# Performance work log

Hardware: AMD Instinct MI355X
Metric: run time of the kernel (lower is better)

## Reference

```python
import jax, jax.numpy as jnp
import numpy as np

B, S, D, H, DFF = 2, 2048, 1024, 16, 4096
DK = D // H
EPS = 1e-6


def setup_inputs() -> dict:
    key = jax.random.key(0)
    ks = jax.random.split(key, 12)
    p = lambda k, shp: (jax.random.normal(k, shp, dtype=jnp.float32) * 0.02)
    return {
        "x": jax.random.normal(ks[0], (B, S, D), dtype=jnp.float32),
        "src_mask": jax.random.randint(ks[1], (B, 1, 1, S), 0, 2, dtype=jnp.int32),
        "wq": p(ks[2], (D, D)), "bq": jnp.zeros((D,), jnp.float32),
        "wk": p(ks[3], (D, D)), "bk": jnp.zeros((D,), jnp.float32),
        "wv": p(ks[4], (D, D)), "bv": jnp.zeros((D,), jnp.float32),
        "wo": p(ks[5], (D, D)), "bo": jnp.zeros((D,), jnp.float32),
        "w1": p(ks[6], (D, DFF)), "b1": jnp.zeros((DFF,), jnp.float32),
        "w2": p(ks[7], (DFF, D)), "b2": jnp.zeros((D,), jnp.float32),
        "a1": jnp.ones((1,), jnp.float32), "g1": jnp.zeros((1,), jnp.float32),
        "a2": jnp.ones((1,), jnp.float32), "g2": jnp.zeros((1,), jnp.float32),
    }


def _layernorm(x, alpha, bias):
    # Faithful to source: scalar alpha/bias, std with Bessel correction, eps on std
    mean = jnp.mean(x, axis=-1, keepdims=True)
    std = jnp.std(x, axis=-1, keepdims=True, ddof=1)
    return alpha * (x - mean) / (std + EPS) + bias


def _encoder_block(x, src_mask, wq, bq, wk, bk, wv, bv, wo, bo,
                   w1, b1, w2, b2, a1, g1, a2, g2):
    # --- self-attention sublayer (pre-norm residual) ---
    n = _layernorm(x, a1, g1)
    q = (n @ wq + bq).reshape(B, S, H, DK)
    k = (n @ wk + bk).reshape(B, S, H, DK)
    v = (n @ wv + bv).reshape(B, S, H, DK)
    scores = jnp.einsum("bqhd,bkhd->bhqk", q, k) / jnp.sqrt(jnp.float32(DK))
    scores = jnp.where(src_mask == 0, jnp.float32(-1e9), scores)
    attn = jax.nn.softmax(scores, axis=-1)
    ctx = jnp.einsum("bhqk,bkhd->bqhd", attn, v).reshape(B, S, D)
    x = x + (ctx @ wo + bo)
    # --- feed-forward sublayer (pre-norm residual) ---
    n2 = _layernorm(x, a2, g2)
    ff = jax.nn.relu(n2 @ w1 + b1) @ w2 + b2
    return x + ff


def reference(x, src_mask, wq, bq, wk, bk, wv, bv, wo, bo,
              w1, b1, w2, b2, a1, g1, a2, g2):
    return _encoder_block(x, src_mask, wq, bq, wk, bk, wv, bv, wo, bo,
                          w1, b1, w2, b2, a1, g1, a2, g2)
```

## Files before the change

kernel.cpp:

```cpp
#include <hip/hip_runtime.h>
#include <hip/hip_bf16.h>
#include <cstdint>

constexpr int Bc  = 2;
constexpr int Sc  = 2048;
constexpr int Dc  = 1024;
constexpr int Hc  = 16;
constexpr int DKc = 64;
constexpr int DFFc= 4096;
constexpr int BSc = Bc * Sc;

typedef __attribute__((ext_vector_type(8))) short bf16x8;
typedef __attribute__((ext_vector_type(4))) float f32x4;

__device__ __forceinline__ unsigned short f2bf(float x){
  union { float f; uint32_t u; } v; v.f = x;
  uint32_t r = v.u + 0x7fffu + ((v.u >> 16) & 1u);
  return (unsigned short)(r >> 16);
}

__device__ __forceinline__ void gload16(const void* g, void* l){
  __builtin_amdgcn_global_load_lds((const __attribute__((address_space(1))) void*)g,
                                   (__attribute__((address_space(3))) void*)l, 16, 0, 0);
}

__device__ __forceinline__ f32x4 mfma16(bf16x8 a, bf16x8 b, f32x4 c){
  return __builtin_amdgcn_mfma_f32_16x16x32_bf16(a, b, c, 0, 0, 0);
}

__device__ __forceinline__ uint32_t pk2bf(float lo, float hi){
  __hip_bfloat162 h = __float22bfloat162_rn(make_float2(lo, hi));
  return *reinterpret_cast<uint32_t*>(&h);
}

__device__ __forceinline__ float fexp2(float x){
  float r; asm("v_exp_f32 %0, %1" : "=v"(r) : "v"(x)); return r;
}

__device__ __forceinline__ int xcd_swz(int bid, int nwg){
  const int q = nwg >> 3, r = nwg & 7;
  const int xcd = bid & 7, idx = bid >> 3;
  return ((xcd < r) ? (xcd * (q + 1)) : (r * (q + 1) + (xcd - r) * q)) + idx;
}

__global__ __launch_bounds__(256)
void prep_all(const float* __restrict__ wq, const float* __restrict__ wk,
              const float* __restrict__ wv, const float* __restrict__ wo,
              const float* __restrict__ w1, const float* __restrict__ w2,
              const float* __restrict__ bq, const float* __restrict__ bk,
              const float* __restrict__ bv,
              unsigned short* __restrict__ wqkv_t, unsigned short* __restrict__ wo_t,
              unsigned short* __restrict__ w1_t, unsigned short* __restrict__ w2_t,
              float* __restrict__ bqkv){
  const int id = blockIdx.x, tid = threadIdx.x;
  if (id >= 12288){
    const int i = (id - 12288) * 256 + tid;
    bqkv[i] = (i < 1024) ? bq[i] : (i < 2048 ? bk[i - 1024] : bv[i - 2048]);
    return;
  }
  const float* in; unsigned short* out; int K, N, bx, by;
  if (id < 4096){
    const int w = id >> 10, local = id & 1023;
    in  = (w == 0) ? wq : (w == 1) ? wk : (w == 2) ? wv : wo;
    out = (w == 0) ? wqkv_t : (w == 1) ? (wqkv_t + 1048576) : (w == 2) ? (wqkv_t + 2097152) : wo_t;
    K = 1024; N = 1024; bx = local & 31; by = local >> 5;
  } else if (id < 8192){
    const int local = id - 4096;
    in = w1; out = w1_t; K = 1024; N = 4096; bx = local & 127; by = local >> 7;
  } else {
    const int local = id - 8192;
    in = w2; out = w2_t; K = 4096; N = 1024; bx = local & 31; by = local >> 5;
  }
  __shared__ float t[32][33];
  const int tx = tid & 31, ty = tid >> 5;
  const int x0 = bx * 32, y0 = by * 32;
#pragma unroll
  for (int j = ty; j < 32; j += 8) t[j][tx] = in[(long)(y0 + j) * N + x0 + tx];
  __syncthreads();
#pragma unroll
  for (int j = ty; j < 32; j += 8)
    out[(long)(x0 + j) * K + y0 + tx] = f2bf(t[tx][j]);
}

__global__ __launch_bounds__(256)
void mask_addend(const int* __restrict__ mask, float* __restrict__ madd){
  int i = blockIdx.x * 256 + threadIdx.x;
  madd[i] = (mask[i] != 0) ? 0.f : -1.442695e9f;
}

__global__ __launch_bounds__(256)
void layernorm_k(const float* __restrict__ x, const float* __restrict__ al,
                 const float* __restrict__ be, unsigned short* __restrict__ out){
  const int row = blockIdx.x, tid = threadIdx.x;
  const float4 v = ((const float4*)(x + (long)row * Dc))[tid];
  float s  = v.x + v.y + v.z + v.w;
  float ss = v.x*v.x + v.y*v.y + v.z*v.z + v.w*v.w;
#pragma unroll
  for (int d = 1; d < 64; d <<= 1){ s += __shfl_xor(s, d, 64); ss += __shfl_xor(ss, d, 64); }
  __shared__ float red[8];
  const int wid = tid >> 6, lane = tid & 63;
  if (lane == 0){ red[wid*2] = s; red[wid*2+1] = ss; }
  __syncthreads();
  s  = red[0] + red[2] + red[4] + red[6];
  ss = red[1] + red[3] + red[5] + red[7];
  const float mean = s * (1.f / 1024.f);
  float var = (ss - s * mean) * (1.f / 1023.f);
  var = fmaxf(var, 0.f);
  const float k = al[0] / (sqrtf(var) + 1e-6f);
  const float g = be[0];
  ushort4 o;
  o.x = f2bf((v.x - mean) * k + g);
  o.y = f2bf((v.y - mean) * k + g);
  o.z = f2bf((v.z - mean) * k + g);
  o.w = f2bf((v.w - mean) * k + g);
  ((ushort4*)(out + (long)row * Dc))[tid] = o;
}

template<int RELU, int OUTBF16, int RES, int VOUT>
__global__ __launch_bounds__(512, 2)
void gemm256(const unsigned short* __restrict__ A, const unsigned short* __restrict__ BT,
             const float* __restrict__ bias, const float* __restrict__ resid,
             void* __restrict__ Cout, unsigned short* __restrict__ vtw,
             int M, int N, int K){
  __shared__ unsigned short As[2][256 * 64];
  __shared__ unsigned short Bs[2][256 * 64];
  const int tid = threadIdx.x, wid = tid >> 6, lane = tid & 63;
  const int lg = lane >> 4, lr = lane & 15;
  const int wm = wid >> 2, wn = wid & 3;
  const int nwg = gridDim.x * gridDim.y;
  const int wg  = xcd_swz(blockIdx.y * gridDim.x + blockIdx.x, nwg);
  const int bx = wg % gridDim.x, by = wg / gridDim.x;
  const int m0 = by * 256, n0 = bx * 256;
  const long ldA = (long)K * 2;
  const f32x4 zero4 = {0.f, 0.f, 0.f, 0.f};
  f32x4 acc[8][4];
#pragma unroll
  for (int i = 0; i < 8; i++)
#pragma unroll
    for (int j = 0; j < 4; j++) acc[i][j] = zero4;

  auto stage_half = [&](int b, int kt, int h){
    const unsigned short* src = (h < 2) ? A : BT;
    const int rowg = ((h < 2) ? m0 : n0) + (h & 1) * 128;
    char* dst = ((h < 2) ? (char*)As[b] : (char*)Bs[b]) + (h & 1) * 16384;
#pragma unroll
    for (int l = 0; l < 2; ++l){
      const int ob = (wid*2 + l) * 1024;
      const int o  = ob + lane * 16;
      const int rr = o >> 7, c = (o >> 4) & 7;
      const long co = (long)kt * 128 + ((c ^ (rr & 7)) << 4);
      gload16((const char*)src + (long)(rowg + rr) * ldA + co, dst + ob);
    }
  };

  const int nt = K >> 6;
#pragma unroll
  for (int h = 0; h < 4; ++h) stage_half(0, 0, h);
  __syncthreads();

  int cur = 0;
  for (int t = 0; t < nt; ++t){
    const char* as = (const char*)As[cur];
    const char* bs = (const char*)Bs[cur];
    bf16x8 bfr[4][2];
#pragma unroll
    for (int p = 0; p < 4; ++p){
      if (p == 0){
#pragma unroll
        for (int ni = 0; ni < 4; ++ni){
          const int row = wn*64 + ni*16 + lr;
#pragma unroll
          for (int ks = 0; ks < 2; ++ks)
            bfr[ni][ks] = *reinterpret_cast<const bf16x8*>(bs + row*128 + (((ks*4 + lg) ^ (row & 7)) << 4));
        }
      }
      bf16x8 af[2][2];
#pragma unroll
      for (int i = 0; i < 2; ++i){
        const int arow = wm*128 + (2*p + i)*16 + lr;
        af[i][0] = *reinterpret_cast<const bf16x8*>(as + arow*128 + (((0*4 + lg) ^ (arow & 7)) << 4));
        af[i][1] = *reinterpret_cast<const bf16x8*>(as + arow*128 + (((1*4 + lg) ^ (arow & 7)) << 4));
      }
      if (t + 1 < nt) stage_half(cur ^ 1, t + 1, p);
      __builtin_amdgcn_sched_barrier(0);
      __builtin_amdgcn_s_barrier();
      asm volatile("s_waitcnt lgkmcnt(0)" ::: "memory");
      __builtin_amdgcn_sched_barrier(0);
      __builtin_amdgcn_s_setprio(1);
#pragma unroll
      for (int i = 0; i < 2; ++i){
        const int mi = 2*p + i;
#pragma unroll
        for (int ni = 0; ni < 4; ++ni){
          acc[mi][ni] = mfma16(af[i][0], bfr[ni][0], acc[mi][ni]);
          acc[mi][ni] = mfma16(af[i][1], bfr[ni][1], acc[mi][ni]);
        }
      }
      __builtin_amdgcn_s_setprio(0);
      __builtin_amdgcn_sched_barrier(0);
      __builtin_amdgcn_s_barrier();
    }
    if (t + 1 < nt){
      asm volatile("s_waitcnt vmcnt(0)" ::: "memory");
      __builtin_amdgcn_s_barrier();
      __builtin_amdgcn_sched_barrier(0);
    }
    cur ^= 1;
  }

  if (VOUT && n0 >= 2048){
#pragma unroll
    for (int mi = 0; mi < 8; ++mi){
      const int row = m0 + wm*128 + mi*16 + lg*4;
      const int b = row >> 11, s = row & 2047;
#pragma unroll
      for (int ni = 0; ni < 4; ++ni){
        const int col = n0 + wn*64 + ni*16 + lr;
        const float bc = bias[col];
        ushort4 o;
        o.x = f2bf(acc[mi][ni][0] + bc);
        o.y = f2bf(acc[mi][ni][1] + bc);
        o.z = f2bf(acc[mi][ni][2] + bc);
        o.w = f2bf(acc[mi][ni][3] + bc);
        *(ushort4*)(vtw + ((long)(b * 1024 + (col - 2048)) << 11) + s) = o;
      }
    }
    return;
  }

#pragma unroll
  for (int mi = 0; mi < 8; ++mi)
#pragma unroll
    for (int ni = 0; ni < 4; ++ni){
      const int col = n0 + wn*64 + ni*16 + lr;
      const float bc = bias[col];
#pragma unroll
      for (int r = 0; r < 4; ++r){
        const int row = m0 + wm*128 + mi*16 + lg*4 + r;
        float v = acc[mi][ni][r] + bc;
        if (RES)  v += resid[(long)row * N + col];
        if (RELU) v = fmaxf(v, 0.f);
        if (OUTBF16) ((unsigned short*)Cout)[(long)row * N + col] = f2bf(v);
        else         ((float*)Cout)[(long)row * N + col] = v;
      }
    }
}

template<int RELU, int OUTBF16, int RES, int PARTIAL>
__global__ __launch_bounds__(512, 2)
void gemm128(const unsigned short* __restrict__ A, const unsigned short* __restrict__ BT,
             const float* __restrict__ bias, const float* __restrict__ resid,
             void* __restrict__ Cout, float* __restrict__ p0,
             float* __restrict__ p1a, float* __restrict__ p1b,
             int M, int N, int K, int ldK){
  __shared__ unsigned short As[2][128 * 64];
  __shared__ unsigned short Bs[2][128 * 64];
  const int tid = threadIdx.x, wid = tid >> 6, lane = tid & 63;
  const int lg = lane >> 4, lr = lane & 15;
  const int wm = wid >> 2, wn = wid & 3;
  const int nwg = gridDim.x * gridDim.y;
  const int wg  = xcd_swz(blockIdx.y * gridDim.x + blockIdx.x, nwg);
  const int bx = wg % gridDim.x, by = wg / gridDim.x;
  const int m0 = by * 128, n0 = bx * 128;
  const int kc = PARTIAL ? blockIdx.z : 0;
  const unsigned short* Ab = A  + (long)kc * K;
  const unsigned short* Bb = BT + (long)kc * K;
  const long ldA = (long)ldK * 2;
  const f32x4 zero4 = {0.f, 0.f, 0.f, 0.f};
  f32x4 acc[4][2];
#pragma unroll
  for (int i = 0; i < 4; i++)
#pragma unroll
    for (int j = 0; j < 2; j++) acc[i][j] = zero4;

  auto stage = [&](int b, int kt){
#pragma unroll
    for (int l = 0; l < 2; ++l){
      const int ob = (wid*2 + l) * 1024;
      const int o  = ob + lane * 16;
      const int rr = o >> 7, c = (o >> 4) & 7;
      const long co = (long)kt * 128 + ((c ^ (rr & 7)) << 4);
      gload16((const char*)Ab + (long)(m0 + rr) * ldA + co, (char*)As[b] + ob);
      gload16((const char*)Bb + (long)(n0 + rr) * ldA + co, (char*)Bs[b] + ob);
    }
  };

  const int nt = K >> 6;
  stage(0, 0);
  stage(1, 1);

  int cur = 0;
  for (int t = 0; t < nt; ++t){
    if (t + 1 < nt) asm volatile("s_waitcnt vmcnt(4)" ::: "memory");
    else            asm volatile("s_waitcnt vmcnt(0)" ::: "memory");
    __builtin_amdgcn_s_barrier();
    __builtin_amdgcn_sched_barrier(0);
    const char* as = (const char*)As[cur];
    const char* bs = (const char*)Bs[cur];
    bf16x8 bfr[2][2];
#pragma unroll
    for (int ni = 0; ni < 2; ++ni){
      const int row = wn*32 + ni*16 + lr;
#pragma unroll
      for (int ks = 0; ks < 2; ++ks)
        bfr[ni][ks] = *reinterpret_cast<const bf16x8*>(bs + row*128 + (((ks*4 + lg) ^ (row & 7)) << 4));
    }
    __builtin_amdgcn_s_setprio(1);
#pragma unroll
    for (int mi = 0; mi < 4; ++mi){
      const int arow = wm*64 + mi*16 + lr;
      bf16x8 a0 = *reinterpret_cast<const bf16x8*>(as + arow*128 + (((0*4 + lg) ^ (arow & 7)) << 4));
      bf16x8 a1 = *reinterpret_cast<const bf16x8*>(as + arow*128 + (((1*4 + lg) ^ (arow & 7)) << 4));
#pragma unroll
      for (int ni = 0; ni < 2; ++ni){
        acc[mi][ni] = mfma16(a0, bfr[ni][0], acc[mi][ni]);
        acc[mi][ni] = mfma16(a1, bfr[ni][1], acc[mi][ni]);
      }
    }
    __builtin_amdgcn_s_setprio(0);
    __builtin_amdgcn_s_barrier();
    __builtin_amdgcn_sched_barrier(0);
    if (t + 2 < nt) stage(cur, t + 2);
    cur ^= 1;
  }

#pragma unroll
  for (int mi = 0; mi < 4; ++mi)
#pragma unroll
    for (int ni = 0; ni < 2; ++ni){
      const int col = n0 + wn*32 + ni*16 + lr;
      float bc = 0.f;
      if (!PARTIAL) bc = bias[col];
#pragma unroll
      for (int r = 0; r < 4; ++r){
        const int row = m0 + wm*64 + mi*16 + lg*4 + r;
        float v = acc[mi][ni][r] + bc;
        if (PARTIAL){
          float* pb = (kc == 0) ? p0 : ((row < 2048) ? p1a : (p1b - 2097152));
          pb[(long)row * N + col] = v;
        } else {
          if (RES)  v += resid[(long)row * N + col];
          if (RELU) v = fmaxf(v, 0.f);
          if (OUTBF16) ((unsigned short*)Cout)[(long)row * N + col] = f2bf(v);
          else         ((float*)Cout)[(long)row * N + col] = v;
        }
      }
    }
}

__global__ __launch_bounds__(256)
void reduce_ff2(const float* __restrict__ p0, const float* __restrict__ p1a,
                const float* __restrict__ p1b, const float* __restrict__ b2,
                float* __restrict__ out){
  const long n4 = (long)BSc * Dc / 4;
  for (long i = (long)blockIdx.x * 256 + threadIdx.x; i < n4; i += (long)gridDim.x * 256){
    const long flat = i * 4;
    const float4 a = ((const float4*)p0)[i];
    const float4 b = (flat < 2097152L) ? ((const float4*)p1a)[i]
                                       : ((const float4*)p1b)[i - 524288L];
    const float4 x = ((const float4*)out)[i];
    const float4 bb = ((const float4*)b2)[(flat & 1023) >> 2];
    float4 r;
    r.x = a.x + b.x + x.x + bb.x;
    r.y = a.y + b.y + x.y + bb.y;
    r.z = a.z + b.z + x.z + bb.z;
    r.w = a.w + b.w + x.w + bb.w;
    ((float4*)out)[i] = r;
  }
}

__global__ __launch_bounds__(512)
void attn_k(const unsigned short* __restrict__ qkv, const unsigned short* __restrict__ vt,
            const float* __restrict__ madd, unsigned short* __restrict__ ctx){
  __shared__ unsigned short Qs[128*64], Ks[2][64*64], Vs[2][64*64], Ps[8*16*64];
  const int tid = threadIdx.x, wid = tid >> 6, lane = tid & 63;
  const int lg = lane >> 4, lr = lane & 15;
  const int f   = blockIdx.y * gridDim.x + blockIdx.x;
  const int xcd = f & 7, j = f >> 3;
  const int bh  = (xcd << 2) | (j & 3);
  const int qt  = j >> 2;
  const int b = bh >> 4, h = bh & 15;
  const int s0 = qt * 128;
  const f32x4 zero4 = {0.f, 0.f, 0.f, 0.f};
  const short onebf = (short)0x3F80;
  const bf16x8 ones = {onebf, onebf, onebf, onebf, onebf, onebf, onebf, onebf};
  const float c1 = 0.18033688f;

  const char* kbase = (const char*)qkv + (long)(b*Sc) * 6144 + 2048 + h * 128;
  const char* vbase = (const char*)vt + (long)bh * 64 * 4096;
  const float* mrow = madd + b * Sc;
  unsigned short* pb = Ps + wid * 1024;

  auto stageKV = [&](int t, int bsel){
    const int o = wid * 1024;
    const int ol = o + lane * 16;
    const int r = ol >> 7, c = (ol >> 4) & 7;
    const int sw = ((c ^ (r & 7)) << 4);
    gload16(kbase + (long)(t*64 + r) * 6144 + sw, (char*)Ks[bsel] + o);
    gload16(vbase + (long)r * 4096 + t*128 + sw, (char*)Vs[bsel] + o);
  };

  const char* qbase = (const char*)qkv + ((long)(b*Sc + s0)) * 6144 + h * 128;
#pragma unroll
  for (int ld = 0; ld < 2; ++ld){
    const int o = (wid*2 + ld) * 1024;
    const int ol = o + lane * 16;
    const int r = ol >> 7, c = (ol >> 4) & 7;
    gload16(qbase + (long)r * 6144 + ((c ^ (r & 7)) << 4), (char*)Qs + o);
  }
  stageKV(0, 0);
  float4 ma[4];
#pragma unroll
  for (int ni = 0; ni < 4; ++ni) ma[ni] = *(const float4*)(mrow + ni*16 + lg*4);
  __syncthreads();
  bf16x8 qb[2];
#pragma unroll
  for (int ks = 0; ks < 2; ++ks){
    const int row = wid*16 + lr;
    qb[ks] = *reinterpret_cast<const bf16x8*>((const char*)Qs + row*128 + (((ks*4 + lg) ^ (row & 7)) << 4));
  }

  f32x4 acc[4] = {zero4, zero4, zero4, zero4};
  f32x4 accS = zero4;
  constexpr int NT = Sc / 64;

  for (int t = 0; t < NT; ++t){
    if (t){
      asm volatile("s_waitcnt vmcnt(0)" ::: "memory");
      __builtin_amdgcn_s_barrier();
      __builtin_amdgcn_sched_barrier(0);
    }
    if (t + 1 < NT) stageKV(t + 1, (t + 1) & 1);
    float4 man[4];
    if (t + 1 < NT){
#pragma unroll
      for (int ni = 0; ni < 4; ++ni) man[ni] = *(const float4*)(mrow + (t+1)*64 + ni*16 + lg*4);
    }

    const int cur = t & 1;
    const char* ksb = (const char*)Ks[cur];
    const char* vsb = (const char*)Vs[cur];

    f32x4 s4[4];
    __builtin_amdgcn_s_setprio(1);
#pragma unroll
    for (int ni = 0; ni < 4; ++ni){
      s4[ni] = zero4;
      const int row = ni*16 + lr;
#pragma unroll
      for (int ks = 0; ks < 2; ++ks){
        bf16x8 ak = *reinterpret_cast<const bf16x8*>(ksb + row*128 + (((ks*4 + lg) ^ (lr & 7)) << 4));
        s4[ni] = mfma16(ak, qb[ks], s4[ni]);
      }
    }
    __builtin_amdgcn_s_setprio(0);

    float p[4][4];
#pragma unroll
    for (int ni = 0; ni < 4; ++ni){
      p[ni][0] = fexp2(fmaf(s4[ni][0], c1, ma[ni].x));
      p[ni][1] = fexp2(fmaf(s4[ni][1], c1, ma[ni].y));
      p[ni][2] = fexp2(fmaf(s4[ni][2], c1, ma[ni].z));
      p[ni][3] = fexp2(fmaf(s4[ni][3], c1, ma[ni].w));
    }

#pragma unroll
    for (int ni = 0; ni < 4; ++ni){
      uint2 w;
      w.x = pk2bf(p[ni][0], p[ni][1]);
      w.y = pk2bf(p[ni][2], p[ni][3]);
      const int c = ni*2 + (lg >> 1);
      char* dst = (char*)pb + lr*128 + ((c ^ (lr & 7)) << 4) + (lg & 1) * 8;
      *(uint2*)dst = w;
    }
    bf16x8 pa[2];
#pragma unroll
    for (int ks = 0; ks < 2; ++ks){
      pa[ks] = *reinterpret_cast<const bf16x8*>((const char*)pb + lr*128 + (((ks*4 + lg) ^ (lr & 7)) << 4));
    }
    __builtin_amdgcn_s_setprio(1);
#pragma unroll
    for (int ks = 0; ks < 2; ++ks) accS = mfma16(pa[ks], ones, accS);
#pragma unroll
    for (int ni = 0; ni < 4; ++ni){
      const int row = ni*16 + lr;
#pragma unroll
      for (int ks = 0; ks < 2; ++ks){
        bf16x8 bv8 = *reinterpret_cast<const bf16x8*>(vsb + row*128 + (((ks*4 + lg) ^ (lr & 7)) << 4));
        acc[ni] = mfma16(pa[ks], bv8, acc[ni]);
      }
    }
    __builtin_amdgcn_s_setprio(0);
    if (t + 1 < NT){
#pragma unroll
      for (int ni = 0; ni < 4; ++ni) ma[ni] = man[ni];
    }
  }
#pragma unroll
  for (int ni = 0; ni < 4; ++ni){
    const int col = h*64 + ni*16 + lr;
#pragma unroll
    for (int r = 0; r < 4; ++r){
      const int row = s0 + wid*16 + lg*4 + r;
      ctx[(long)(b*Sc + row) * Dc + col] = f2bf(acc[ni][r] / accS[r]);
    }
  }
}

extern "C" void kernel_launch(void* const* d_in, const int* in_sizes, int n_in,
                              void* d_out, int out_size, void* d_ws, size_t ws_size,
                              hipStream_t stream){
  const float* x  = (const float*)d_in[0];
  const int* mask = (const int*)d_in[1];
  const float* wq = (const float*)d_in[2];
  const float* bq = (const float*)d_in[3];
  const float* wk = (const float*)d_in[4];
  const float* bk = (const float*)d_in[5];
  const float* wv = (const float*)d_in[6];
  const float* bv = (const float*)d_in[7];
  const float* wo = (const float*)d_in[8];
  const float* bo = (const float*)d_in[9];
  const float* w1 = (const float*)d_in[10];
  const float* b1 = (const float*)d_in[11];
  const float* w2 = (const float*)d_in[12];
  const float* b2 = (const float*)d_in[13];
  const float* a1 = (const float*)d_in[14];
  const float* g1 = (const float*)d_in[15];
  const float* a2 = (const float*)d_in[16];
  const float* g2 = (const float*)d_in[17];

  if (ws_size < 75509760u) return;

  char* ws = (char*)d_ws;
  unsigned short* wqkv_t = (unsigned short*)(ws + 0);
  unsigned short* wo_t   = (unsigned short*)(ws + 6291456);
  unsigned short* w1_t   = (unsigned short*)(ws + 8388608);
  unsigned short* w2_t   = (unsigned short*)(ws + 16777216);
  float*          bqkv   = (float*)(ws + 25165824);
  unsigned short* nbuf   = (unsigned short*)(ws + 25178112);
  float*          maddf  = (float*)(ws + 25178112);
  unsigned short* qkv    = (unsigned short*)(ws + 33566720);
  unsigned short* ff1    = (unsigned short*)(ws + 33566720);
  unsigned short* vt     = (unsigned short*)(ws + 58732544);
  unsigned short* ctx    = (unsigned short*)(ws + 67121152);
  float* p0  = (float*)(ws + 0);
  float* p1a = (float*)(ws + 25178112);
  float* p1b = (float*)(ws + 67121152);
  float* x2 = (float*)d_out;

  prep_all<<<12300, 256, 0, stream>>>(wq, wk, wv, wo, w1, w2, bq, bk, bv,
                                      wqkv_t, wo_t, w1_t, w2_t, bqkv);

  layernorm_k<<<BSc, 256, 0, stream>>>(x, a1, g1, nbuf);
  gemm256<0,1,0,1><<<dim3(12, 16), 512, 0, stream>>>(nbuf, wqkv_t, bqkv, nullptr, qkv, vt, BSc, 3072, 1024);
  mask_addend<<<16, 256, 0, stream>>>(mask, maddf);
  attn_k<<<dim3(16, 32), 512, 0, stream>>>(qkv, vt, maddf, ctx);
  gemm128<0,0,1,0><<<dim3(8, 32), 512, 0, stream>>>(ctx, wo_t, bo, x, x2,
                                                    nullptr, nullptr, nullptr, BSc, 1024, 1024, 1024);
  layernorm_k<<<BSc, 256, 0, stream>>>(x2, a2, g2, nbuf);
  gemm256<1,1,0,0><<<dim3(16, 16), 512, 0, stream>>>(nbuf, w1_t, b1, nullptr, ff1, nullptr, BSc, 4096, 1024);
  gemm128<0,0,0,1><<<dim3(8, 32, 2), 512, 0, stream>>>(ff1, w2_t, nullptr, nullptr, nullptr,
                                                       p0, p1a, p1b, BSc, 1024, 2048, 4096);
  reduce_ff2<<<2048, 256, 0, stream>>>(p0, p1a, p1b, b2, (float*)d_out);
}
```

Baseline: 222.4 us.

## Use 128x64 tiles for N=1024 GEMMs and drop split-K FF2 reduction

The 128x128 GEMM kernel is replaced by a 128x64-tile variant, so the output-projection and FF2 GEMMs each launch 512 workgroups instead of 256. FF2 no longer splits K into two partial buffers followed by a separate reduce kernel. It runs the full K=4096 in one pass and fuses bias and residual into the epilogue, reading the residual in place from the output buffer. This removes the partial-sum write and re-read traffic and one kernel launch. In exchange each wave computes a smaller 32x32 sub-tile, which lowers LDS and MFMA reuse per load, and FF2 blocks now run a longer K loop.

```diff
diff --git a/kernel.cpp b/kernel.cpp
--- a/kernel.cpp
+++ b/kernel.cpp
@@ -246,30 +246,25 @@
     }
 }
 
-template<int RELU, int OUTBF16, int RES, int PARTIAL>
+template<int RELU, int OUTBF16, int RES>
 __global__ __launch_bounds__(512, 2)
-void gemm128(const unsigned short* __restrict__ A, const unsigned short* __restrict__ BT,
-             const float* __restrict__ bias, const float* __restrict__ resid,
-             void* __restrict__ Cout, float* __restrict__ p0,
-             float* __restrict__ p1a, float* __restrict__ p1b,
-             int M, int N, int K, int ldK){
+void gemm12864(const unsigned short* __restrict__ A, const unsigned short* __restrict__ BT,
+               const float* __restrict__ bias, const float* __restrict__ resid,
+               void* __restrict__ Cout, int M, int N, int K){
   __shared__ unsigned short As[2][128 * 64];
-  __shared__ unsigned short Bs[2][128 * 64];
+  __shared__ unsigned short Bs[2][64 * 64];
   const int tid = threadIdx.x, wid = tid >> 6, lane = tid & 63;
   const int lg = lane >> 4, lr = lane & 15;
-  const int wm = wid >> 2, wn = wid & 3;
+  const int wm = wid >> 1, wn = wid & 1;
   const int nwg = gridDim.x * gridDim.y;
   const int wg  = xcd_swz(blockIdx.y * gridDim.x + blockIdx.x, nwg);
   const int bx = wg % gridDim.x, by = wg / gridDim.x;
-  const int m0 = by * 128, n0 = bx * 128;
-  const int kc = PARTIAL ? blockIdx.z : 0;
-  const unsigned short* Ab = A  + (long)kc * K;
-  const unsigned short* Bb = BT + (long)kc * K;
-  const long ldA = (long)ldK * 2;
+  const int m0 = by * 128, n0 = bx * 64;
+  const long ldA = (long)K * 2;
   const f32x4 zero4 = {0.f, 0.f, 0.f, 0.f};
-  f32x4 acc[4][2];
-#pragma unroll
-  for (int i = 0; i < 4; i++)
+  f32x4 acc[2][2];
+#pragma unroll
+  for (int i = 0; i < 2; i++)
 #pragma unroll
     for (int j = 0; j < 2; j++) acc[i][j] = zero4;
 
@@ -280,8 +275,14 @@
       const int o  = ob + lane * 16;
       const int rr = o >> 7, c = (o >> 4) & 7;
       const long co = (long)kt * 128 + ((c ^ (rr & 7)) << 4);
-      gload16((const char*)Ab + (long)(m0 + rr) * ldA + co, (char*)As[b] + ob);
-      gload16((const char*)Bb + (long)(n0 + rr) * ldA + co, (char*)Bs[b] + ob);
+      gload16((const char*)A + (long)(m0 + rr) * ldA + co, (char*)As[b] + ob);
+    }
+    {
+      const int ob = wid * 1024;
+      const int o  = ob + lane * 16;
+      const int rr = o >> 7, c = (o >> 4) & 7;
+      const long co = (long)kt * 128 + ((c ^ (rr & 7)) << 4);
+      gload16((const char*)BT + (long)(n0 + rr) * ldA + co, (char*)Bs[b] + ob);
     }
   };
 
@@ -291,7 +292,7 @@
 
   int cur = 0;
   for (int t = 0; t < nt; ++t){
-    if (t + 1 < nt) asm volatile("s_waitcnt vmcnt(4)" ::: "memory");
+    if (t + 1 < nt) asm volatile("s_waitcnt vmcnt(3)" ::: "memory");
     else            asm volatile("s_waitcnt vmcnt(0)" ::: "memory");
     __builtin_amdgcn_s_barrier();
     __builtin_amdgcn_sched_barrier(0);
@@ -307,8 +308,8 @@
     }
     __builtin_amdgcn_s_setprio(1);
 #pragma unroll
-    for (int mi = 0; mi < 4; ++mi){
-      const int arow = wm*64 + mi*16 + lr;
+    for (int mi = 0; mi < 2; ++mi){
+      const int arow = wm*32 + mi*16 + lr;
       bf16x8 a0 = *reinterpret_cast<const bf16x8*>(as + arow*128 + (((0*4 + lg) ^ (arow & 7)) << 4));
       bf16x8 a1 = *reinterpret_cast<const bf16x8*>(as + arow*128 + (((1*4 + lg) ^ (arow & 7)) << 4));
 #pragma unroll
@@ -325,48 +326,21 @@
   }
 
 #pragma unroll
-  for (int mi = 0; mi < 4; ++mi)
+  for (int mi = 0; mi < 2; ++mi)
 #pragma unroll
     for (int ni = 0; ni < 2; ++ni){
       const int col = n0 + wn*32 + ni*16 + lr;
-      float bc = 0.f;
-      if (!PARTIAL) bc = bias[col];
+      const float bc = bias[col];
 #pragma unroll
       for (int r = 0; r < 4; ++r){
-        const int row = m0 + wm*64 + mi*16 + lg*4 + r;
+        const int row = m0 + wm*32 + mi*16 + lg*4 + r;
         float v = acc[mi][ni][r] + bc;
-        if (PARTIAL){
-          float* pb = (kc == 0) ? p0 : ((row < 2048) ? p1a : (p1b - 2097152));
-          pb[(long)row * N + col] = v;
-        } else {
-          if (RES)  v += resid[(long)row * N + col];
-          if (RELU) v = fmaxf(v, 0.f);
-          if (OUTBF16) ((unsigned short*)Cout)[(long)row * N + col] = f2bf(v);
-          else         ((float*)Cout)[(long)row * N + col] = v;
-        }
-      }
-    }
-}
-
-__global__ __launch_bounds__(256)
-void reduce_ff2(const float* __restrict__ p0, const float* __restrict__ p1a,
-                const float* __restrict__ p1b, const float* __restrict__ b2,
-                float* __restrict__ out){
-  const long n4 = (long)BSc * Dc / 4;
-  for (long i = (long)blockIdx.x * 256 + threadIdx.x; i < n4; i += (long)gridDim.x * 256){
-    const long flat = i * 4;
-    const float4 a = ((const float4*)p0)[i];
-    const float4 b = (flat < 2097152L) ? ((const float4*)p1a)[i]
-                                       : ((const float4*)p1b)[i - 524288L];
-    const float4 x = ((const float4*)out)[i];
-    const float4 bb = ((const float4*)b2)[(flat & 1023) >> 2];
-    float4 r;
-    r.x = a.x + b.x + x.x + bb.x;
-    r.y = a.y + b.y + x.y + bb.y;
-    r.z = a.z + b.z + x.z + bb.z;
-    r.w = a.w + b.w + x.w + bb.w;
-    ((float4*)out)[i] = r;
-  }
+        if (RES)  v += resid[(long)row * N + col];
+        if (RELU) v = fmaxf(v, 0.f);
+        if (OUTBF16) ((unsigned short*)Cout)[(long)row * N + col] = f2bf(v);
+        else         ((float*)Cout)[(long)row * N + col] = v;
+      }
+    }
 }
 
 __global__ __launch_bounds__(512)
@@ -543,9 +517,6 @@
   unsigned short* ff1    = (unsigned short*)(ws + 33566720);
   unsigned short* vt     = (unsigned short*)(ws + 58732544);
   unsigned short* ctx    = (unsigned short*)(ws + 67121152);
-  float* p0  = (float*)(ws + 0);
-  float* p1a = (float*)(ws + 25178112);
-  float* p1b = (float*)(ws + 67121152);
   float* x2 = (float*)d_out;
 
   prep_all<<<12300, 256, 0, stream>>>(wq, wk, wv, wo, w1, w2, bq, bk, bv,
@@ -555,11 +526,8 @@
   gemm256<0,1,0,1><<<dim3(12, 16), 512, 0, stream>>>(nbuf, wqkv_t, bqkv, nullptr, qkv, vt, BSc, 3072, 1024);
   mask_addend<<<16, 256, 0, stream>>>(mask, maddf);
   attn_k<<<dim3(16, 32), 512, 0, stream>>>(qkv, vt, maddf, ctx);
-  gemm128<0,0,1,0><<<dim3(8, 32), 512, 0, stream>>>(ctx, wo_t, bo, x, x2,
-                                                    nullptr, nullptr, nullptr, BSc, 1024, 1024, 1024);
+  gemm12864<0,0,1><<<dim3(16, 32), 512, 0, stream>>>(ctx, wo_t, bo, x, x2, BSc, 1024, 1024);
   layernorm_k<<<BSc, 256, 0, stream>>>(x2, a2, g2, nbuf);
   gemm256<1,1,0,0><<<dim3(16, 16), 512, 0, stream>>>(nbuf, w1_t, b1, nullptr, ff1, nullptr, BSc, 4096, 1024);
-  gemm128<0,0,0,1><<<dim3(8, 32, 2), 512, 0, stream>>>(ff1, w2_t, nullptr, nullptr, nullptr,
-                                                       p0, p1a, p1b, BSc, 1024, 2048, 4096);
-  reduce_ff2<<<2048, 256, 0, stream>>>(p0, p1a, p1b, b2, (float*)d_out);
-}
+  gemm12864<0,0,1><<<dim3(16, 32), 512, 0, stream>>>(ff1, w2_t, b2, x2, d_out, BSc, 1024, 4096);
+}
```

Result: no change. 220.5 us (-0.8%).
